# Optimization experiments

Measured on AMD Instinct MI355X. Metric: run time of the kernel, lower is better.

Reference implementation:

```python
import jax, jax.numpy as jnp
import numpy as np

DIM = 2048
N_HEADS = 32
N_KV_HEADS = 8
HEAD_DIM = DIM // N_HEADS  # 64
N_REP = N_HEADS // N_KV_HEADS
ROPE_BASE = 10000.0


def rope_tables(seq_len, dim):
    inv_freq = 1.0 / (ROPE_BASE ** (jnp.arange(0, dim, 2, dtype=jnp.float32) / dim))
    t = jnp.arange(seq_len, dtype=jnp.float32)
    freqs = jnp.outer(t, inv_freq)            # [S, dim/2]
    emb = jnp.concatenate([freqs, freqs], -1)  # [S, dim]
    return jnp.cos(emb), jnp.sin(emb)          # each [S, dim]


def rotate_half(x):
    x1, x2 = jnp.split(x, 2, axis=-1)
    return jnp.concatenate([-x2, x1], axis=-1)


def setup_inputs() -> dict:
    key = jax.random.key(0)
    k_x, k_q, k_k, k_v, k_o = jax.random.split(key, 5)
    B, S = 2, 2048
    scale = 0.02
    x = jax.random.normal(k_x, (B, S, DIM), dtype=jnp.float32)
    # torch Linear weights are [out, in]
    w_q = jax.random.normal(k_q, (N_HEADS * HEAD_DIM, DIM), dtype=jnp.float32) * scale
    w_k = jax.random.normal(k_k, (N_KV_HEADS * HEAD_DIM, DIM), dtype=jnp.float32) * scale
    w_v = jax.random.normal(k_v, (N_KV_HEADS * HEAD_DIM, DIM), dtype=jnp.float32) * scale
    w_o = jax.random.normal(k_o, (DIM, N_HEADS * HEAD_DIM), dtype=jnp.float32) * scale
    return {"x": x, "w_q": w_q, "w_k": w_k, "w_v": w_v, "w_o": w_o}


def reference(x, w_q, w_k, w_v, w_o):
    B, S, _ = x.shape
    # projections (torch Linear: x @ W^T), reshape to [B, H, S, D]
    q = jnp.einsum('bsd,ed->bse', x, w_q).reshape(B, S, N_HEADS, HEAD_DIM).transpose(0, 2, 1, 3)
    k = jnp.einsum('bsd,ed->bse', x, w_k).reshape(B, S, N_KV_HEADS, HEAD_DIM).transpose(0, 2, 1, 3)
    v = jnp.einsum('bsd,ed->bse', x, w_v).reshape(B, S, N_KV_HEADS, HEAD_DIM).transpose(0, 2, 1, 3)
    # RoPE
    cos, sin = rope_tables(S, HEAD_DIM)  # [S, D]
    cos = cos[None, None]
    sin = sin[None, None]
    q = q * cos + rotate_half(q) * sin
    k = k * cos + rotate_half(k) * sin
    # GQA: expand kv heads (repeat_interleave along head dim)
    k = jnp.repeat(k, N_REP, axis=1)
    v = jnp.repeat(v, N_REP, axis=1)
    # attention
    scores = jnp.einsum('bhqd,bhkd->bhqk', q, k) / jnp.sqrt(jnp.float32(HEAD_DIM))
    attn = jax.nn.softmax(scores, axis=-1)
    out = jnp.einsum('bhqk,bhkd->bhqd', attn, v)
    out = out.transpose(0, 2, 1, 3).reshape(B, S, N_HEADS * HEAD_DIM)
    return jnp.einsum('bse,de->bsd', out, w_o)
```

## Files before the change

### kernel.cpp

```cpp
#include <hip/hip_runtime.h>
#include <hip/hip_bf16.h>

typedef __attribute__((ext_vector_type(8))) short bf16x8;
typedef __attribute__((ext_vector_type(4))) short bf16x4s;
typedef __attribute__((ext_vector_type(4))) float f32x4;
typedef __attribute__((ext_vector_type(2))) unsigned int u32x2;
typedef unsigned int u32;

#define DIM 2048
#define NH 32
#define NKV 8
#define HD 64
#define BB 2
#define SS 2048
#define MROWS (BB*SS)
#define NQKV 3072
#define KDIM 2048
#define L2E 1.44269504f

__device__ __forceinline__ short f2bf(float f){
  u32 u = __float_as_uint(f);
  u32 r = u + 0x7fffu + ((u >> 16) & 1u);
  return (short)(r >> 16);
}
__device__ __forceinline__ float bf2f(short s){
  return __uint_as_float(((u32)(unsigned short)s) << 16);
}

__device__ __forceinline__ void gload16(const void* g, void* l){
  __builtin_amdgcn_global_load_lds((const __attribute__((address_space(1))) u32*)g,
                                   (__attribute__((address_space(3))) u32*)l, 16, 0, 0);
}

__global__ __launch_bounds__(256) void cvt_all_kernel(const float* __restrict__ x,
                                                      const float* __restrict__ wq,
                                                      const float* __restrict__ wk,
                                                      const float* __restrict__ wv,
                                                      const float* __restrict__ wo,
                                                      short* __restrict__ xb,
                                                      short* __restrict__ wqkvb,
                                                      short* __restrict__ wob){
  int bid = blockIdx.x;
  int i = bid*256 + threadIdx.x;
  const float* src; short* dst; int off;
  if      (bid <  8192){ src = x;  dst = xb;              off = 0; }
  else if (bid < 12288){ src = wq; dst = wqkvb;           off = 2097152; }
  else if (bid < 13312){ src = wk; dst = wqkvb+2048*2048; off = 3145728; }
  else if (bid < 14336){ src = wv; dst = wqkvb+2560*2048; off = 3407872; }
  else                 { src = wo; dst = wob;             off = 3670016; }
  int j = i - off;
  f32x4 v = ((const f32x4*)src)[j];
  bf16x4s o;
  #pragma unroll
  for (int t=0;t<4;++t) o[t] = f2bf(v[t]);
  ((bf16x4s*)dst)[j] = o;
}

__global__ __launch_bounds__(256) void ropetab_kernel(float* __restrict__ cosT,
                                                      float* __restrict__ sinT){
  int idx = blockIdx.x*256 + threadIdx.x;
  if (idx >= SS*32) return;
  int s = idx >> 5, i = idx & 31;
  float inv = powf(10000.f, -(float)i * (1.f/32.f));
  float f = (float)s * inv;
  cosT[idx] = cosf(f);
  sinT[idx] = sinf(f);
}

__global__ __launch_bounds__(256) void vT_kernel(const short* __restrict__ qkv,
                                                 short* __restrict__ Vtg){
  __shared__ short T[64*72];
  const int tid = threadIdx.x;
  const int s0 = blockIdx.x*64, hkv = blockIdx.y, b = blockIdx.z;
  const short* vbase = qkv + (size_t)b*SS*NQKV + DIM + NKV*HD + hkv*HD;
  #pragma unroll
  for (int cc=0; cc<2; ++cc){
    int c = tid + cc*256;
    int s = c >> 3, dc = c & 7;
    bf16x8 v = *(const bf16x8*)(vbase + (size_t)(s0+s)*NQKV + dc*8);
    #pragma unroll
    for (int i=0;i<8;++i) T[(dc*8+i)*72 + s] = v[i];
  }
  __syncthreads();
  short* obase = Vtg + ((size_t)(b*NKV + hkv)*64)*SS;
  #pragma unroll
  for (int cc=0; cc<2; ++cc){
    int c = tid + cc*256;
    int d = c >> 3, sc = c & 7;
    *(bf16x8*)(obase + (size_t)d*SS + s0 + sc*8) = *(const bf16x8*)&T[d*72 + sc*8];
  }
}

__global__ __launch_bounds__(256) void gemm_bt_kernel(const short* __restrict__ A,
                                                      const short* __restrict__ Bm,
                                                      short* __restrict__ C,
                                                      int ldc, int K,
                                                      const float* __restrict__ cosT,
                                                      const float* __restrict__ sinT,
                                                      int rope){
  __shared__ short As[128*32];
  __shared__ short Bs[128*32];
  const int tid = threadIdx.x;
  const int wave = tid >> 6, lane = tid & 63;
  const int g = lane >> 4, r16 = lane & 15;
  const int m0 = blockIdx.y * 128, n0 = blockIdx.x * 128;
  const int wr = wave >> 1, wc = wave & 1;
  f32x4 acc[4][4] = {};
  for (int k0 = 0; k0 < K; k0 += 32){
    #pragma unroll
    for (int c2 = 0; c2 < 2; ++c2){
      int ch = (wave*2 + c2)*64 + lane;
      int row = ch >> 2, kc = ch & 3;
      gload16(A  + (size_t)(m0+row)*K + k0 + kc*8, (char*)As + (wave*2+c2)*1024);
      gload16(Bm + (size_t)(n0+row)*K + k0 + kc*8, (char*)Bs + (wave*2+c2)*1024);
    }
    __syncthreads();
    bf16x8 a[4], b[4];
    #pragma unroll
    for (int i=0;i<4;++i)
      a[i] = *(const bf16x8*)&As[(wr*64 + i*16 + r16)*32 + g*8];
    #pragma unroll
    for (int j=0;j<4;++j)
      b[j] = *(const bf16x8*)&Bs[(wc*64 + j*16 + r16)*32 + g*8];
    #pragma unroll
    for (int i=0;i<4;++i)
      #pragma unroll
      for (int j=0;j<4;++j)
        acc[i][j] = __builtin_amdgcn_mfma_f32_16x16x32_bf16(a[i], b[j], acc[i][j], 0, 0, 0);
    __syncthreads();
  }
  if (rope && n0 < 2560){
    float qsc = (n0 < 2048) ? 0.125f : 1.0f;
    #pragma unroll
    for (int i=0;i<4;++i)
      #pragma unroll
      for (int r=0;r<4;++r){
        int row = m0 + wr*64 + i*16 + g*4 + r;
        int s = row & (SS-1);
        #pragma unroll
        for (int j=0;j<2;++j){
          int col = n0 + wc*64 + j*16 + r16;
          float c  = cosT[(s<<5) + (col&31)];
          float sn = sinT[(s<<5) + (col&31)];
          float x1 = acc[i][j][r], x2 = acc[i][j+2][r];
          C[(size_t)row*ldc + col]      = f2bf((x1*c - x2*sn)*qsc);
          C[(size_t)row*ldc + col + 32] = f2bf((x2*c + x1*sn)*qsc);
        }
      }
  } else {
    #pragma unroll
    for (int i=0;i<4;++i)
      #pragma unroll
      for (int j=0;j<4;++j)
        #pragma unroll
        for (int r=0;r<4;++r){
          int row = m0 + wr*64 + i*16 + g*4 + r;
          int col = n0 + wc*64 + j*16 + r16;
          C[(size_t)row*ldc + col] = f2bf(acc[i][j][r]);
        }
  }
}

__global__ __launch_bounds__(256) void gemm_btf_kernel(const short* __restrict__ A,
                                                       const short* __restrict__ Bm,
                                                       float* __restrict__ C,
                                                       int ldc, int K){
  __shared__ short As[128*32];
  __shared__ short Bs[128*32];
  const int tid = threadIdx.x;
  const int wave = tid >> 6, lane = tid & 63;
  const int g = lane >> 4, r16 = lane & 15;
  const int m0 = blockIdx.y * 128, n0 = blockIdx.x * 128;
  const int wr = wave >> 1, wc = wave & 1;
  f32x4 acc[4][4] = {};
  for (int k0 = 0; k0 < K; k0 += 32){
    #pragma unroll
    for (int c2 = 0; c2 < 2; ++c2){
      int ch = (wave*2 + c2)*64 + lane;
      int row = ch >> 2, kc = ch & 3;
      gload16(A  + (size_t)(m0+row)*K + k0 + kc*8, (char*)As + (wave*2+c2)*1024);
      gload16(Bm + (size_t)(n0+row)*K + k0 + kc*8, (char*)Bs + (wave*2+c2)*1024);
    }
    __syncthreads();
    bf16x8 a[4], b[4];
    #pragma unroll
    for (int i=0;i<4;++i)
      a[i] = *(const bf16x8*)&As[(wr*64 + i*16 + r16)*32 + g*8];
    #pragma unroll
    for (int j=0;j<4;++j)
      b[j] = *(const bf16x8*)&Bs[(wc*64 + j*16 + r16)*32 + g*8];
    #pragma unroll
    for (int i=0;i<4;++i)
      #pragma unroll
      for (int j=0;j<4;++j)
        acc[i][j] = __builtin_amdgcn_mfma_f32_16x16x32_bf16(a[i], b[j], acc[i][j], 0, 0, 0);
    __syncthreads();
  }
  #pragma unroll
  for (int i=0;i<4;++i)
    #pragma unroll
    for (int j=0;j<4;++j)
      #pragma unroll
      for (int r=0;r<4;++r){
        int row = m0 + wr*64 + i*16 + g*4 + r;
        int col = n0 + wc*64 + j*16 + r16;
        C[(size_t)row*ldc + col] = acc[i][j][r];
      }
}

__global__ __launch_bounds__(512) void attn_kernel(const short* __restrict__ qkv,
                                                   const short* __restrict__ Vtg,
                                                   short* __restrict__ outb){
  __shared__ short Ks[128*64];
  __shared__ short Vt[64*128];
  __shared__ short Ps[8*16*72];
  const int tid = threadIdx.x;
  const int wave = tid >> 6, lane = tid & 63;
  const int g = lane >> 4, r16 = lane & 15;
  const int qt = blockIdx.x, h = blockIdx.y, b = blockIdx.z;
  const int hkv = h >> 2;
  const size_t row0 = (size_t)b * SS;
  const int qrow0 = qt*128 + wave*16;
  const short* qbase  = qkv + (row0 + qrow0)*NQKV + h*HD;
  const short* kbase  = qkv + row0*NQKV + DIM + hkv*HD;
  const short* vtbase = Vtg + ((size_t)(b*NKV + hkv)*64)*SS;

  bf16x8 qf[2];
  #pragma unroll
  for (int kk=0;kk<2;++kk)
    qf[kk] = *(const bf16x8*)(qbase + (size_t)r16*NQKV + kk*32 + g*8);

  f32x4 oaccT[4] = {};
  float M = -6.0e29f;
  float lrow = 0.f;

  short* pwv = &Ps[wave*16*72];

  for (int s0 = 0; s0 < SS; s0 += 128){
    #pragma unroll
    for (int c=0;c<2;++c){
      int ch = tid + c*512;
      int krow = ch >> 3, c3 = ch & 7;
      gload16(kbase + (size_t)(s0+krow)*NQKV + ((c3 ^ (krow&7)) << 3),
              (char*)Ks + c*8192 + wave*1024);
      int d = ch >> 4, c16 = ch & 15;
      gload16(vtbase + (size_t)d*SS + s0 + ((c16 ^ (d&15)) << 3),
              (char*)Vt + c*8192 + wave*1024);
    }
    __syncthreads();

    f32x4 sacc[8];
    #pragma unroll
    for (int t=0;t<8;++t){
      f32x4 cacc = {};
      #pragma unroll
      for (int kk=0;kk<2;++kk){
        int krow = t*16 + r16;
        const bf16x8* kp = (const bf16x8*)((const char*)Ks + krow*128 +
                            ((((kk<<2)+g) ^ (krow&7)) << 4));
        cacc = __builtin_amdgcn_mfma_f32_16x16x32_bf16(*kp, qf[kk], cacc, 0,0,0);
      }
      sacc[t] = cacc;
    }

    float mx = sacc[0][0];
    #pragma unroll
    for (int t=0;t<8;++t)
      #pragma unroll
      for (int r=0;r<4;++r) mx = fmaxf(mx, sacc[t][r]);
    mx = fmaxf(mx, __shfl_xor(mx, 16));
    mx = fmaxf(mx, __shfl_xor(mx, 32));
    float mxl = mx * L2E;
    if (__any(mxl > M + 11.5f)){
      float Mnew = fmaxf(M, mxl);
      float al;
      { float a = M - Mnew; asm("v_exp_f32 %0, %1" : "=v"(al) : "v"(a)); }
      lrow *= al;
      #pragma unroll
      for (int j=0;j<4;++j)
        #pragma unroll
        for (int r=0;r<4;++r) oaccT[j][r] *= al;
      M = Mnew;
    }
    float sum = 0.f;
    u32 pb[8][2];
    #pragma unroll
    for (int t=0;t<8;++t){
      float p[4];
      #pragma unroll
      for (int r=0;r<4;++r){
        float a = fmaf(sacc[t][r], L2E, -M);
        asm("v_exp_f32 %0, %1" : "=v"(p[r]) : "v"(a));
        sum += p[r];
      }
      asm("v_cvt_pk_bf16_f32 %0, %1, %2" : "=v"(pb[t][0]) : "v"(p[0]), "v"(p[1]));
      asm("v_cvt_pk_bf16_f32 %0, %1, %2" : "=v"(pb[t][1]) : "v"(p[2]), "v"(p[3]));
    }
    sum += __shfl_xor(sum, 16);
    sum += __shfl_xor(sum, 32);
    lrow += sum;

    #pragma unroll
    for (int h2=0;h2<2;++h2){
      #pragma unroll
      for (int t2=0;t2<4;++t2)
        *(u32x2*)&pwv[r16*72 + t2*16 + g*4] = (u32x2){pb[h2*4+t2][0], pb[h2*4+t2][1]};
      #pragma unroll
      for (int kki=0;kki<2;++kki){
        bf16x8 pf = *(const bf16x8*)&pwv[r16*72 + 32*kki + g*8];
        int kkg = h2*2 + kki;
        #pragma unroll
        for (int j=0;j<4;++j){
          int d = j*16 + r16;
          const bf16x8* vp = (const bf16x8*)((const char*)Vt + d*256 +
                              ((((kkg<<2)+g) ^ (d&15)) << 4));
          oaccT[j] = __builtin_amdgcn_mfma_f32_16x16x32_bf16(*vp, pf, oaccT[j], 0,0,0);
        }
      }
    }
    __syncthreads();
  }

  float inv = 1.0f / lrow;
  short* orow = outb + (row0 + qrow0 + r16)*(size_t)DIM + h*HD;
  #pragma unroll
  for (int j=0;j<4;++j){
    bf16x4s ov;
    #pragma unroll
    for (int r=0;r<4;++r) ov[r] = f2bf(oaccT[j][r]*inv);
    *(bf16x4s*)&orow[j*16 + g*4] = ov;
  }
}

extern "C" void kernel_launch(void* const* d_in, const int* in_sizes, int n_in,
                              void* d_out, int out_size, void* d_ws, size_t ws_size,
                              hipStream_t stream){
  const float* x  = (const float*)d_in[0];
  const float* wq = (const float*)d_in[1];
  const float* wk = (const float*)d_in[2];
  const float* wv = (const float*)d_in[3];
  const float* wo = (const float*)d_in[4];
  float* outf = (float*)d_out;

  char* ws = (char*)d_ws;
  short* wqkvb = (short*)(ws);
  short* attnb = (short*)(ws);
  short* wob   = (short*)(ws + 16777216);
  short* qkv   = (short*)(ws + 25165824);
  float* cosT  = (float*)(ws + 50331648);
  float* sinT  = (float*)(ws + 50593792);
  short* xb    = (short*)d_out;
  short* Vtg   = (short*)((char*)d_out + 16777216);

  cvt_all_kernel<<<18432, 256, 0, stream>>>(x, wq, wk, wv, wo, xb, wqkvb, wob);
  ropetab_kernel<<<256, 256, 0, stream>>>(cosT, sinT);

  gemm_bt_kernel<<<dim3(NQKV/128, MROWS/128), 256, 0, stream>>>(xb, wqkvb, qkv, NQKV, KDIM,
                                                                cosT, sinT, 1);
  vT_kernel<<<dim3(SS/64, NKV, BB), 256, 0, stream>>>(qkv, Vtg);
  attn_kernel<<<dim3(SS/128, NH, BB), 512, 0, stream>>>(qkv, Vtg, attnb);
  gemm_btf_kernel<<<dim3(DIM/128, MROWS/128), 256, 0, stream>>>(attnb, wob, outf, DIM, KDIM);
}
```

Baseline: 251.2 us.

## Double-buffer GEMM and attention LDS tiles, fold RoPE table into convert kernel

Both bf16 GEMM kernels now use two LDS buffers: the next K-slice is issued with global_load_lds while MFMAs run on the current one, leaving one barrier per iteration instead of two. The attention kernel is double-buffered the same way, with its key tile cut from 128 to 64 so both buffers fit in LDS, and the swizzles adjusted to match. The RoPE cos/sin table work moves into extra blocks of the conversion kernel, which removes one launch. In exchange, LDS use per GEMM block doubles, which may lower occupancy. The smaller attention tile also means more loop iterations and barriers per query block.

```diff
diff --git a/kernel.cpp b/kernel.cpp
--- a/kernel.cpp
+++ b/kernel.cpp
@@ -39,8 +39,19 @@
                                                       const float* __restrict__ wo,
                                                       short* __restrict__ xb,
                                                       short* __restrict__ wqkvb,
-                                                      short* __restrict__ wob){
+                                                      short* __restrict__ wob,
+                                                      float* __restrict__ cosT,
+                                                      float* __restrict__ sinT){
   int bid = blockIdx.x;
+  if (bid >= 18432){
+    int idx = (bid-18432)*256 + threadIdx.x;
+    int s = idx >> 5, i = idx & 31;
+    float inv = powf(10000.f, -(float)i * (1.f/32.f));
+    float f = (float)s * inv;
+    cosT[idx] = cosf(f);
+    sinT[idx] = sinf(f);
+    return;
+  }
   int i = bid*256 + threadIdx.x;
   const float* src; short* dst; int off;
   if      (bid <  8192){ src = x;  dst = xb;              off = 0; }
@@ -56,17 +67,6 @@
   ((bf16x4s*)dst)[j] = o;
 }
 
-__global__ __launch_bounds__(256) void ropetab_kernel(float* __restrict__ cosT,
-                                                      float* __restrict__ sinT){
-  int idx = blockIdx.x*256 + threadIdx.x;
-  if (idx >= SS*32) return;
-  int s = idx >> 5, i = idx & 31;
-  float inv = powf(10000.f, -(float)i * (1.f/32.f));
-  float f = (float)s * inv;
-  cosT[idx] = cosf(f);
-  sinT[idx] = sinf(f);
-}
-
 __global__ __launch_bounds__(256) void vT_kernel(const short* __restrict__ qkv,
                                                  short* __restrict__ Vtg){
   __shared__ short T[64*72];
@@ -98,37 +98,48 @@
                                                       const float* __restrict__ cosT,
                                                       const float* __restrict__ sinT,
                                                       int rope){
-  __shared__ short As[128*32];
-  __shared__ short Bs[128*32];
+  __shared__ short As[2][128*32];
+  __shared__ short Bs[2][128*32];
   const int tid = threadIdx.x;
   const int wave = tid >> 6, lane = tid & 63;
   const int g = lane >> 4, r16 = lane & 15;
   const int m0 = blockIdx.y * 128, n0 = blockIdx.x * 128;
   const int wr = wave >> 1, wc = wave & 1;
   f32x4 acc[4][4] = {};
-  for (int k0 = 0; k0 < K; k0 += 32){
+
+  auto STAGE = [&](int k0, int bufi){
     #pragma unroll
     for (int c2 = 0; c2 < 2; ++c2){
       int ch = (wave*2 + c2)*64 + lane;
       int row = ch >> 2, kc = ch & 3;
-      gload16(A  + (size_t)(m0+row)*K + k0 + kc*8, (char*)As + (wave*2+c2)*1024);
-      gload16(Bm + (size_t)(n0+row)*K + k0 + kc*8, (char*)Bs + (wave*2+c2)*1024);
-    }
-    __syncthreads();
+      gload16(A  + (size_t)(m0+row)*K + k0 + kc*8, (char*)&As[bufi][0] + (wave*2+c2)*1024);
+      gload16(Bm + (size_t)(n0+row)*K + k0 + kc*8, (char*)&Bs[bufi][0] + (wave*2+c2)*1024);
+    }
+  };
+
+  STAGE(0, 0);
+  __syncthreads();
+
+  int bb = 0;
+  for (int k0 = 0; k0 < K; k0 += 32){
+    bool more = (k0 + 32 < K);
+    if (more) STAGE(k0+32, bb^1);
     bf16x8 a[4], b[4];
     #pragma unroll
     for (int i=0;i<4;++i)
-      a[i] = *(const bf16x8*)&As[(wr*64 + i*16 + r16)*32 + g*8];
+      a[i] = *(const bf16x8*)&As[bb][(wr*64 + i*16 + r16)*32 + g*8];
     #pragma unroll
     for (int j=0;j<4;++j)
-      b[j] = *(const bf16x8*)&Bs[(wc*64 + j*16 + r16)*32 + g*8];
+      b[j] = *(const bf16x8*)&Bs[bb][(wc*64 + j*16 + r16)*32 + g*8];
     #pragma unroll
     for (int i=0;i<4;++i)
       #pragma unroll
       for (int j=0;j<4;++j)
         acc[i][j] = __builtin_amdgcn_mfma_f32_16x16x32_bf16(a[i], b[j], acc[i][j], 0, 0, 0);
-    __syncthreads();
-  }
+    if (more) __syncthreads();
+    bb ^= 1;
+  }
+
   if (rope && n0 < 2560){
     float qsc = (n0 < 2048) ? 0.125f : 1.0f;
     #pragma unroll
@@ -165,36 +176,46 @@
                                                        const short* __restrict__ Bm,
                                                        float* __restrict__ C,
                                                        int ldc, int K){
-  __shared__ short As[128*32];
-  __shared__ short Bs[128*32];
+  __shared__ short As[2][128*32];
+  __shared__ short Bs[2][128*32];
   const int tid = threadIdx.x;
   const int wave = tid >> 6, lane = tid & 63;
   const int g = lane >> 4, r16 = lane & 15;
   const int m0 = blockIdx.y * 128, n0 = blockIdx.x * 128;
   const int wr = wave >> 1, wc = wave & 1;
   f32x4 acc[4][4] = {};
-  for (int k0 = 0; k0 < K; k0 += 32){
+
+  auto STAGE = [&](int k0, int bufi){
     #pragma unroll
     for (int c2 = 0; c2 < 2; ++c2){
       int ch = (wave*2 + c2)*64 + lane;
       int row = ch >> 2, kc = ch & 3;
-      gload16(A  + (size_t)(m0+row)*K + k0 + kc*8, (char*)As + (wave*2+c2)*1024);
-      gload16(Bm + (size_t)(n0+row)*K + k0 + kc*8, (char*)Bs + (wave*2+c2)*1024);
-    }
-    __syncthreads();
+      gload16(A  + (size_t)(m0+row)*K + k0 + kc*8, (char*)&As[bufi][0] + (wave*2+c2)*1024);
+      gload16(Bm + (size_t)(n0+row)*K + k0 + kc*8, (char*)&Bs[bufi][0] + (wave*2+c2)*1024);
+    }
+  };
+
+  STAGE(0, 0);
+  __syncthreads();
+
+  int bb = 0;
+  for (int k0 = 0; k0 < K; k0 += 32){
+    bool more = (k0 + 32 < K);
+    if (more) STAGE(k0+32, bb^1);
     bf16x8 a[4], b[4];
     #pragma unroll
     for (int i=0;i<4;++i)
-      a[i] = *(const bf16x8*)&As[(wr*64 + i*16 + r16)*32 + g*8];
+      a[i] = *(const bf16x8*)&As[bb][(wr*64 + i*16 + r16)*32 + g*8];
     #pragma unroll
     for (int j=0;j<4;++j)
-      b[j] = *(const bf16x8*)&Bs[(wc*64 + j*16 + r16)*32 + g*8];
+      b[j] = *(const bf16x8*)&Bs[bb][(wc*64 + j*16 + r16)*32 + g*8];
     #pragma unroll
     for (int i=0;i<4;++i)
       #pragma unroll
       for (int j=0;j<4;++j)
         acc[i][j] = __builtin_amdgcn_mfma_f32_16x16x32_bf16(a[i], b[j], acc[i][j], 0, 0, 0);
-    __syncthreads();
+    if (more) __syncthreads();
+    bb ^= 1;
   }
   #pragma unroll
   for (int i=0;i<4;++i)
@@ -211,8 +232,8 @@
 __global__ __launch_bounds__(512) void attn_kernel(const short* __restrict__ qkv,
                                                    const short* __restrict__ Vtg,
                                                    short* __restrict__ outb){
-  __shared__ short Ks[128*64];
-  __shared__ short Vt[64*128];
+  __shared__ short Ks[2][64*64];
+  __shared__ short Vt[2][64*64];
   __shared__ short Ps[8*16*72];
   const int tid = threadIdx.x;
   const int wave = tid >> 6, lane = tid & 63;
@@ -236,38 +257,46 @@
 
   short* pwv = &Ps[wave*16*72];
 
-  for (int s0 = 0; s0 < SS; s0 += 128){
-    #pragma unroll
-    for (int c=0;c<2;++c){
-      int ch = tid + c*512;
-      int krow = ch >> 3, c3 = ch & 7;
-      gload16(kbase + (size_t)(s0+krow)*NQKV + ((c3 ^ (krow&7)) << 3),
-              (char*)Ks + c*8192 + wave*1024);
-      int d = ch >> 4, c16 = ch & 15;
-      gload16(vtbase + (size_t)d*SS + s0 + ((c16 ^ (d&15)) << 3),
-              (char*)Vt + c*8192 + wave*1024);
-    }
-    __syncthreads();
-
-    f32x4 sacc[8];
-    #pragma unroll
-    for (int t=0;t<8;++t){
+  auto STAGE = [&](int s0, int bufi){
+    int key = tid >> 3, c3 = tid & 7;
+    gload16(kbase + (size_t)(s0+key)*NQKV + ((c3 ^ (key&7)) << 3),
+            (char*)&Ks[bufi][0] + wave*1024);
+    int d = tid >> 3;
+    gload16(vtbase + (size_t)d*SS + s0 + ((c3 ^ (d&7)) << 3),
+            (char*)&Vt[bufi][0] + wave*1024);
+  };
+
+  STAGE(0, 0);
+  __syncthreads();
+
+  int buf = 0;
+  const int NT = SS/64;
+  for (int t = 0; t < NT; ++t){
+    bool more = (t+1 < NT);
+    if (more) STAGE((t+1)*64, buf^1);
+
+    const char* ksb = (const char*)&Ks[buf][0];
+    const char* vtb = (const char*)&Vt[buf][0];
+
+    f32x4 sacc[4];
+    #pragma unroll
+    for (int t2=0;t2<4;++t2){
       f32x4 cacc = {};
       #pragma unroll
       for (int kk=0;kk<2;++kk){
-        int krow = t*16 + r16;
-        const bf16x8* kp = (const bf16x8*)((const char*)Ks + krow*128 +
+        int krow = t2*16 + r16;
+        const bf16x8* kp = (const bf16x8*)(ksb + krow*128 +
                             ((((kk<<2)+g) ^ (krow&7)) << 4));
         cacc = __builtin_amdgcn_mfma_f32_16x16x32_bf16(*kp, qf[kk], cacc, 0,0,0);
       }
-      sacc[t] = cacc;
-    }
-
-    float mx = sacc[0][0];
-    #pragma unroll
-    for (int t=0;t<8;++t)
-      #pragma unroll
-      for (int r=0;r<4;++r) mx = fmaxf(mx, sacc[t][r]);
+      sacc[t2] = cacc;
+    }
+
+    float m01 = fmaxf(fmaxf(sacc[0][0], sacc[0][1]), fmaxf(sacc[0][2], sacc[0][3]));
+    float m23 = fmaxf(fmaxf(sacc[1][0], sacc[1][1]), fmaxf(sacc[1][2], sacc[1][3]));
+    float m45 = fmaxf(fmaxf(sacc[2][0], sacc[2][1]), fmaxf(sacc[2][2], sacc[2][3]));
+    float m67 = fmaxf(fmaxf(sacc[3][0], sacc[3][1]), fmaxf(sacc[3][2], sacc[3][3]));
+    float mx = fmaxf(fmaxf(m01, m23), fmaxf(m45, m67));
     mx = fmaxf(mx, __shfl_xor(mx, 16));
     mx = fmaxf(mx, __shfl_xor(mx, 32));
     float mxl = mx * L2E;
@@ -282,43 +311,42 @@
         for (int r=0;r<4;++r) oaccT[j][r] *= al;
       M = Mnew;
     }
-    float sum = 0.f;
-    u32 pb[8][2];
-    #pragma unroll
-    for (int t=0;t<8;++t){
+    float s4[4] = {0.f,0.f,0.f,0.f};
+    u32 pb[4][2];
+    #pragma unroll
+    for (int t2=0;t2<4;++t2){
       float p[4];
       #pragma unroll
       for (int r=0;r<4;++r){
-        float a = fmaf(sacc[t][r], L2E, -M);
+        float a = fmaf(sacc[t2][r], L2E, -M);
         asm("v_exp_f32 %0, %1" : "=v"(p[r]) : "v"(a));
-        sum += p[r];
-      }
-      asm("v_cvt_pk_bf16_f32 %0, %1, %2" : "=v"(pb[t][0]) : "v"(p[0]), "v"(p[1]));
-      asm("v_cvt_pk_bf16_f32 %0, %1, %2" : "=v"(pb[t][1]) : "v"(p[2]), "v"(p[3]));
-    }
+        s4[r] += p[r];
+      }
+      asm("v_cvt_pk_bf16_f32 %0, %1, %2" : "=v"(pb[t2][0]) : "v"(p[0]), "v"(p[1]));
+      asm("v_cvt_pk_bf16_f32 %0, %1, %2" : "=v"(pb[t2][1]) : "v"(p[2]), "v"(p[3]));
+    }
+    float sum = (s4[0]+s4[1]) + (s4[2]+s4[3]);
     sum += __shfl_xor(sum, 16);
     sum += __shfl_xor(sum, 32);
     lrow += sum;
 
     #pragma unroll
-    for (int h2=0;h2<2;++h2){
-      #pragma unroll
-      for (int t2=0;t2<4;++t2)
-        *(u32x2*)&pwv[r16*72 + t2*16 + g*4] = (u32x2){pb[h2*4+t2][0], pb[h2*4+t2][1]};
-      #pragma unroll
-      for (int kki=0;kki<2;++kki){
-        bf16x8 pf = *(const bf16x8*)&pwv[r16*72 + 32*kki + g*8];
-        int kkg = h2*2 + kki;
-        #pragma unroll
-        for (int j=0;j<4;++j){
-          int d = j*16 + r16;
-          const bf16x8* vp = (const bf16x8*)((const char*)Vt + d*256 +
-                              ((((kkg<<2)+g) ^ (d&15)) << 4));
-          oaccT[j] = __builtin_amdgcn_mfma_f32_16x16x32_bf16(*vp, pf, oaccT[j], 0,0,0);
-        }
-      }
-    }
-    __syncthreads();
+    for (int t2=0;t2<4;++t2)
+      *(u32x2*)&pwv[r16*72 + t2*16 + g*4] = (u32x2){pb[t2][0], pb[t2][1]};
+    #pragma unroll
+    for (int kki=0;kki<2;++kki){
+      bf16x8 pf = *(const bf16x8*)&pwv[r16*72 + 32*kki + g*8];
+      #pragma unroll
+      for (int j=0;j<4;++j){
+        int d = j*16 + r16;
+        const bf16x8* vp = (const bf16x8*)(vtb + d*128 +
+                            ((((kki<<2)+g) ^ (d&7)) << 4));
+        oaccT[j] = __builtin_amdgcn_mfma_f32_16x16x32_bf16(*vp, pf, oaccT[j], 0,0,0);
+      }
+    }
+
+    if (more) __syncthreads();
+    buf ^= 1;
   }
 
   float inv = 1.0f / lrow;
@@ -352,8 +380,7 @@
   short* xb    = (short*)d_out;
   short* Vtg   = (short*)((char*)d_out + 16777216);
 
-  cvt_all_kernel<<<18432, 256, 0, stream>>>(x, wq, wk, wv, wo, xb, wqkvb, wob);
-  ropetab_kernel<<<256, 256, 0, stream>>>(cosT, sinT);
+  cvt_all_kernel<<<18688, 256, 0, stream>>>(x, wq, wk, wv, wo, xb, wqkvb, wob, cosT, sinT);
 
   gemm_bt_kernel<<<dim3(NQKV/128, MROWS/128), 256, 0, stream>>>(xb, wqkvb, qkv, NQKV, KDIM,
                                                                 cosT, sinT, 1);
```

New measurement: 304.4 us. 21.2% more time.
